# Kernel optimization log

Hardware: AMD Instinct MI355X
Metric: run time of the kernel (lower is better)

Reference implementation:

```python
import jax, jax.numpy as jnp
import numpy as np

V, DW, DH, OUT = 50000, 300, 50, 4
B, T = 1024, 200


def setup_inputs() -> dict:
    key = jax.random.key(0)
    ks = jax.random.split(key, 9)
    x = jax.random.randint(ks[0], (B, T), 0, V)
    lengs = jax.random.randint(ks[1], (B,), 1, T + 1)  # valid lengths >= 1
    k = 1.0 / np.sqrt(DH)
    emb = jax.random.normal(ks[2], (V, DW), jnp.float32)
    emb = emb.at[0].set(0.0)  # padding_idx=0
    w_ih = jax.random.uniform(ks[3], (4 * DH, DW), jnp.float32, -k, k)
    w_hh = jax.random.uniform(ks[4], (4 * DH, DH), jnp.float32, -k, k)
    b_ih = jax.random.uniform(ks[5], (4 * DH,), jnp.float32, -k, k)
    b_hh = jax.random.uniform(ks[6], (4 * DH,), jnp.float32, -k, k)
    w_out = jax.random.uniform(ks[7], (OUT, DH), jnp.float32, -k, k)
    b_out = jax.random.uniform(ks[8], (OUT,), jnp.float32, -k, k)
    return {"x": x, "lengs": lengs, "emb": emb, "w_ih": w_ih, "w_hh": w_hh,
            "b_ih": b_ih, "b_hh": b_hh, "w_out": w_out, "b_out": b_out}


def reference(x, lengs, emb, w_ih, w_hh, b_ih, b_hh, w_out, b_out):
    b, t = x.shape
    xe = emb[x]                                        # [B,T,DW]
    mask = jnp.arange(t)[None, :] < lengs[:, None]     # [B,T] valid steps
    bias = b_ih + b_hh                                 # [4*DH]

    def step(carry, inp):
        h, c = carry
        x_t, m_t = inp                                 # [B,DW], [B]
        g = x_t @ w_ih.T + h @ w_hh.T + bias           # [B,4*DH]
        i, f, gg, o = jnp.split(g, 4, axis=-1)         # torch gate order i,f,g,o
        c_new = jax.nn.sigmoid(f) * c + jax.nn.sigmoid(i) * jnp.tanh(gg)
        h_new = jax.nn.sigmoid(o) * jnp.tanh(c_new)
        m = m_t[:, None]
        # packed-sequence semantics: state frozen past each sequence's length
        return (jnp.where(m, h_new, h), jnp.where(m, c_new, c)), None

    h0 = jnp.zeros((b, DH), xe.dtype)
    (h, _), _ = jax.lax.scan(step, (h0, h0),
                             (xe.transpose(1, 0, 2), mask.T))
    logits = h @ w_out.T + b_out                       # hidden.view(B,-1) -> Linear
    return jax.nn.softmax(logits, axis=1)
```

## Files before the change

### kernel.cpp

```cpp
#include <hip/hip_runtime.h>
#include <math.h>

#define VOCAB 50000
#define DW 300
#define DH 50
#define G4 200
#define BATCH 1024
#define TMAX 200
#define OUTC 4

__global__ __launch_bounds__(256) void transpose_wih(
    const float* __restrict__ w_ih, float* __restrict__ w_T)
{
    int i = blockIdx.x * 256 + threadIdx.x;
    if (i < G4 * DW) {
        int u = i / DW, k = i % DW;
        w_T[k * G4 + u] = w_ih[i];
    }
}

__global__ __launch_bounds__(256, 2) void proj_kernel(
    const float* __restrict__ emb, const float* __restrict__ w_T,
    const float* __restrict__ b_ih, const float* __restrict__ b_hh,
    float* __restrict__ emb_proj)
{
    __shared__ __align__(16) float e_s[100 * 108];
    const int tid = threadIdx.x;
    const int v0 = blockIdx.x * 100;
    const int m_idx = tid / 25;
    const int n_idx = tid % 25;

    float acc[10][8];
#pragma unroll
    for (int m = 0; m < 10; m++)
#pragma unroll
        for (int c = 0; c < 8; c++) acc[m][c] = 0.f;

    for (int kc = 0; kc < DW; kc += 100) {
        __syncthreads();
        for (int i = tid; i < 2500; i += 256) {
            int r = i / 25, c = i % 25;
            float4 v = *(const float4*)&emb[(size_t)(v0 + r) * DW + kc + c * 4];
            *(float4*)&e_s[r * 108 + c * 4] = v;
        }
        __syncthreads();

        if (tid < 250) {
#pragma unroll 2
            for (int kk = 0; kk < 25; kk++) {
                float4 e4[10];
#pragma unroll
                for (int m = 0; m < 10; m++)
                    e4[m] = *(const float4*)&e_s[(m_idx * 10 + m) * 108 + kk * 4];
                const float* wbase = w_T + (size_t)(kc + kk * 4) * G4 + n_idx * 8;
#pragma unroll
                for (int j = 0; j < 4; j++) {
                    float4 wa = *(const float4*)(wbase + j * G4);
                    float4 wb = *(const float4*)(wbase + j * G4 + 4);
#pragma unroll
                    for (int m = 0; m < 10; m++) {
                        float ev = (j == 0) ? e4[m].x : (j == 1) ? e4[m].y
                                 : (j == 2) ? e4[m].z : e4[m].w;
                        acc[m][0] = fmaf(ev, wa.x, acc[m][0]);
                        acc[m][1] = fmaf(ev, wa.y, acc[m][1]);
                        acc[m][2] = fmaf(ev, wa.z, acc[m][2]);
                        acc[m][3] = fmaf(ev, wa.w, acc[m][3]);
                        acc[m][4] = fmaf(ev, wb.x, acc[m][4]);
                        acc[m][5] = fmaf(ev, wb.y, acc[m][5]);
                        acc[m][6] = fmaf(ev, wb.z, acc[m][6]);
                        acc[m][7] = fmaf(ev, wb.w, acc[m][7]);
                    }
                }
            }
        }
    }

    if (tid < 250) {
#pragma unroll
        for (int c = 0; c < 8; c++) {
            int u = n_idx * 8 + c;
            float bias = b_ih[u] + b_hh[u];
            int u2 = (u % DH) * 4 + (u / DH);
#pragma unroll
            for (int m = 0; m < 10; m++)
                emb_proj[(size_t)(v0 + m_idx * 10 + m) * G4 + u2] = acc[m][c] + bias;
        }
    }
}

__device__ __forceinline__ float tanh_f(float x) {
    float e2 = __expf(fminf(2.f * x, 60.f));
    return (e2 - 1.f) / (e2 + 1.f);
}

__global__ __launch_bounds__(64, 1) void lstm_kernel(
    const int* __restrict__ x, const int* __restrict__ lengs,
    const float* __restrict__ emb_proj, const float* __restrict__ w_hh,
    const float* __restrict__ w_out, const float* __restrict__ b_out,
    float* __restrict__ out)
{
    __shared__ __align__(16) float h_s[52];
    __shared__ int x_s[TMAX];
    __shared__ float red[OUTC];

    const int l  = threadIdx.x;
    const int b  = blockIdx.x;
    const int ll = (l < DH) ? l : DH - 1;
    const int len = lengs[b];

    for (int i = l; i < TMAX; i += 64) x_s[i] = x[b * TMAX + i];
    if (l < 52) h_s[l] = 0.f;

    float4 rwi[13], rwf[13], rwg[13], rwo[13];
    {
        const float* wr;
#define LOADROW(dst, gate)                                                    \
        wr = w_hh + (size_t)((gate) * DH + ll) * DH;                          \
        _Pragma("unroll")                                                     \
        for (int k4 = 0; k4 < 12; k4++) {                                     \
            float2 a = *(const float2*)(wr + 4 * k4);                         \
            float2 bb = *(const float2*)(wr + 4 * k4 + 2);                    \
            dst[k4] = make_float4(a.x, a.y, bb.x, bb.y);                      \
        }                                                                     \
        { float2 a = *(const float2*)(wr + 48);                               \
          dst[12] = make_float4(a.x, a.y, 0.f, 0.f); }
        LOADROW(rwi, 0) LOADROW(rwf, 1) LOADROW(rwg, 2) LOADROW(rwo, 3)
#undef LOADROW
    }

    float c_reg = 0.f;
    const float* ep = emb_proj;
    float4 p0 = *(const float4*)(ep + (size_t)x_s[0] * G4 + 4 * ll);
    float4 p1 = *(const float4*)(ep + (size_t)x_s[1 < TMAX ? 1 : 0] * G4 + 4 * ll);

    for (int t = 0; t < len; t++) {
        float4 cur = p0;
        p0 = p1;
        int nt = (t + 2 < TMAX) ? t + 2 : TMAX - 1;
        p1 = *(const float4*)(ep + (size_t)x_s[nt] * G4 + 4 * ll);

        float gi = cur.x, gf = cur.y, gc = cur.z, go = cur.w;
#pragma unroll
        for (int k4 = 0; k4 < 13; k4++) {
            float4 h4 = *(const float4*)&h_s[4 * k4];
            gi = fmaf(h4.x, rwi[k4].x, fmaf(h4.y, rwi[k4].y,
                 fmaf(h4.z, rwi[k4].z, fmaf(h4.w, rwi[k4].w, gi))));
            gf = fmaf(h4.x, rwf[k4].x, fmaf(h4.y, rwf[k4].y,
                 fmaf(h4.z, rwf[k4].z, fmaf(h4.w, rwf[k4].w, gf))));
            gc = fmaf(h4.x, rwg[k4].x, fmaf(h4.y, rwg[k4].y,
                 fmaf(h4.z, rwg[k4].z, fmaf(h4.w, rwg[k4].w, gc))));
            go = fmaf(h4.x, rwo[k4].x, fmaf(h4.y, rwo[k4].y,
                 fmaf(h4.z, rwo[k4].z, fmaf(h4.w, rwo[k4].w, go))));
        }
        float si = 1.f / (1.f + __expf(-gi));
        float sf = 1.f / (1.f + __expf(-gf));
        float so = 1.f / (1.f + __expf(-go));
        float cn = fmaf(sf, c_reg, si * tanh_f(gc));
        c_reg = cn;
        float hn = so * tanh_f(cn);
        if (l < DH) h_s[l] = hn;
    }

    if (l < OUTC) {
        float lg = b_out[l];
        const float* wo = w_out + l * DH;
#pragma unroll
        for (int k = 0; k < DH; k++) lg = fmaf(h_s[k], wo[k], lg);
        red[l] = lg;
    }
    if (l < OUTC) {
        float m = fmaxf(fmaxf(red[0], red[1]), fmaxf(red[2], red[3]));
        float s = 0.f;
#pragma unroll
        for (int j = 0; j < OUTC; j++) s += __expf(red[j] - m);
        out[b * OUTC + l] = __expf(red[l] - m) / s;
    }
}

extern "C" void kernel_launch(void* const* d_in, const int* in_sizes, int n_in,
                              void* d_out, int out_size, void* d_ws, size_t ws_size,
                              hipStream_t stream) {
    const int*   x     = (const int*)d_in[0];
    const int*   lengs = (const int*)d_in[1];
    const float* emb   = (const float*)d_in[2];
    const float* w_ih  = (const float*)d_in[3];
    const float* w_hh  = (const float*)d_in[4];
    const float* b_ih  = (const float*)d_in[5];
    const float* b_hh  = (const float*)d_in[6];
    const float* w_out = (const float*)d_in[7];
    const float* b_out = (const float*)d_in[8];
    float* out = (float*)d_out;

    float* emb_proj = (float*)d_ws;
    float* w_T      = emb_proj + (size_t)VOCAB * G4;

    hipLaunchKernelGGL(transpose_wih, dim3((G4 * DW + 255) / 256), dim3(256),
                       0, stream, w_ih, w_T);
    hipLaunchKernelGGL(proj_kernel, dim3(VOCAB / 100), dim3(256), 0, stream,
                       emb, w_T, b_ih, b_hh, emb_proj);
    hipLaunchKernelGGL(lstm_kernel, dim3(BATCH), dim3(64), 0, stream,
                       x, lengs, emb_proj, w_hh, w_out, b_out, out);
}
```

Baseline: 353.9 us.

## Broadcast LSTM hidden state via readlane and register-pipeline the projection GEMM

The recurrent loop now keeps h in registers and broadcasts each element with readlane, replacing the LDS write and read of h every timestep. The loop is unrolled by two with predicated updates instead of an exact-length loop. The projection GEMM drops its LDS staging and syncthreads, loads embedding rows and weights straight from global memory with double-buffered registers, and uses 80-row tiles. W_hh is also pre-laid-out into padded float4 rows by a merged prep kernel. These changes trade LDS traffic for more register pressure and more uncoalesced global loads in the GEMM.

```diff
diff --git a/kernel.cpp b/kernel.cpp
--- a/kernel.cpp
+++ b/kernel.cpp
@@ -9,14 +9,59 @@
 #define TMAX 200
 #define OUTC 4
 
-__global__ __launch_bounds__(256) void transpose_wih(
-    const float* __restrict__ w_ih, float* __restrict__ w_T)
+
+__global__ __launch_bounds__(256) void prep_kernel(
+    const float* __restrict__ w_ih, const float* __restrict__ w_hh,
+    float* __restrict__ w_T, float* __restrict__ w2)
 {
     int i = blockIdx.x * 256 + threadIdx.x;
     if (i < G4 * DW) {
         int u = i / DW, k = i % DW;
         w_T[k * G4 + u] = w_ih[i];
     }
+    int j = i - G4 * DW;
+    if (j >= 0 && j < DH * 208) {
+        int l = j / 208, r = j % 208;
+        int g = r / 52, k = r % 52;
+        w2[j] = (k < DH) ? w_hh[(g * DH + l) * DH + k] : 0.f;
+    }
+}
+
+__device__ __forceinline__ float getc(const float4& v, int kc) {
+    return kc == 0 ? v.x : kc == 1 ? v.y : kc == 2 ? v.z : v.w;
+}
+
+__device__ __forceinline__ void loade(const float* eb, int kk, float4 (&e)[8]) {
+#pragma unroll
+    for (int m = 0; m < 8; m++)
+        e[m] = *(const float4*)(eb + m * DW + kk * 4);
+}
+__device__ __forceinline__ void loadw(const float* wb, int kk,
+                                      float4 (&wa)[4], float4 (&wb4)[4]) {
+#pragma unroll
+    for (int j = 0; j < 4; j++) {
+        wa[j]  = *(const float4*)(wb + (kk * 4 + j) * G4);
+        wb4[j] = *(const float4*)(wb + (kk * 4 + j) * G4 + 4);
+    }
+}
+__device__ __forceinline__ void comp8(const float4 (&e)[8],
+                                      const float4 (&wa)[4], const float4 (&wb4)[4],
+                                      float (&acc)[8][8]) {
+#pragma unroll
+    for (int j = 0; j < 4; j++) {
+#pragma unroll
+        for (int m = 0; m < 8; m++) {
+            float ev = getc(e[m], j);
+            acc[m][0] = fmaf(ev, wa[j].x,  acc[m][0]);
+            acc[m][1] = fmaf(ev, wa[j].y,  acc[m][1]);
+            acc[m][2] = fmaf(ev, wa[j].z,  acc[m][2]);
+            acc[m][3] = fmaf(ev, wa[j].w,  acc[m][3]);
+            acc[m][4] = fmaf(ev, wb4[j].x, acc[m][4]);
+            acc[m][5] = fmaf(ev, wb4[j].y, acc[m][5]);
+            acc[m][6] = fmaf(ev, wb4[j].z, acc[m][6]);
+            acc[m][7] = fmaf(ev, wb4[j].w, acc[m][7]);
+        }
+    }
 }
 
 __global__ __launch_bounds__(256, 2) void proj_kernel(
@@ -24,67 +69,39 @@
     const float* __restrict__ b_ih, const float* __restrict__ b_hh,
     float* __restrict__ emb_proj)
 {
-    __shared__ __align__(16) float e_s[100 * 108];
     const int tid = threadIdx.x;
-    const int v0 = blockIdx.x * 100;
-    const int m_idx = tid / 25;
-    const int n_idx = tid % 25;
-
-    float acc[10][8];
-#pragma unroll
-    for (int m = 0; m < 10; m++)
+    const int tt  = (tid < 250) ? tid : 249;
+    const int m_idx = tt / 25, n_idx = tt % 25;
+    const int r0 = blockIdx.x * 80 + m_idx * 8;
+
+    const float* eb = emb + (size_t)r0 * DW;
+    const float* wb = w_T + n_idx * 8;
+
+    float acc[8][8];
+#pragma unroll
+    for (int m = 0; m < 8; m++)
 #pragma unroll
         for (int c = 0; c < 8; c++) acc[m][c] = 0.f;
 
-    for (int kc = 0; kc < DW; kc += 100) {
-        __syncthreads();
-        for (int i = tid; i < 2500; i += 256) {
-            int r = i / 25, c = i % 25;
-            float4 v = *(const float4*)&emb[(size_t)(v0 + r) * DW + kc + c * 4];
-            *(float4*)&e_s[r * 108 + c * 4] = v;
-        }
-        __syncthreads();
-
-        if (tid < 250) {
-#pragma unroll 2
-            for (int kk = 0; kk < 25; kk++) {
-                float4 e4[10];
-#pragma unroll
-                for (int m = 0; m < 10; m++)
-                    e4[m] = *(const float4*)&e_s[(m_idx * 10 + m) * 108 + kk * 4];
-                const float* wbase = w_T + (size_t)(kc + kk * 4) * G4 + n_idx * 8;
-#pragma unroll
-                for (int j = 0; j < 4; j++) {
-                    float4 wa = *(const float4*)(wbase + j * G4);
-                    float4 wb = *(const float4*)(wbase + j * G4 + 4);
-#pragma unroll
-                    for (int m = 0; m < 10; m++) {
-                        float ev = (j == 0) ? e4[m].x : (j == 1) ? e4[m].y
-                                 : (j == 2) ? e4[m].z : e4[m].w;
-                        acc[m][0] = fmaf(ev, wa.x, acc[m][0]);
-                        acc[m][1] = fmaf(ev, wa.y, acc[m][1]);
-                        acc[m][2] = fmaf(ev, wa.z, acc[m][2]);
-                        acc[m][3] = fmaf(ev, wa.w, acc[m][3]);
-                        acc[m][4] = fmaf(ev, wb.x, acc[m][4]);
-                        acc[m][5] = fmaf(ev, wb.y, acc[m][5]);
-                        acc[m][6] = fmaf(ev, wb.z, acc[m][6]);
-                        acc[m][7] = fmaf(ev, wb.w, acc[m][7]);
-                    }
-                }
-            }
-        }
-    }
-
-    if (tid < 250) {
-#pragma unroll
-        for (int c = 0; c < 8; c++) {
-            int u = n_idx * 8 + c;
-            float bias = b_ih[u] + b_hh[u];
-            int u2 = (u % DH) * 4 + (u / DH);
-#pragma unroll
-            for (int m = 0; m < 10; m++)
-                emb_proj[(size_t)(v0 + m_idx * 10 + m) * G4 + u2] = acc[m][c] + bias;
-        }
+    float4 eC[8], eN[8], wCa[4], wCb[4], wNa[4], wNb[4];
+    loade(eb, 0, eC); loadw(wb, 0, wCa, wCb);
+
+    for (int k4 = 0; k4 < 74; k4 += 2) {
+        loade(eb, k4 + 1, eN); loadw(wb, k4 + 1, wNa, wNb);
+        comp8(eC, wCa, wCb, acc);
+        loade(eb, k4 + 2, eC); loadw(wb, k4 + 2, wCa, wCb);
+        comp8(eN, wNa, wNb, acc);
+    }
+    comp8(eC, wCa, wCb, acc);
+
+#pragma unroll
+    for (int c = 0; c < 8; c++) {
+        int u = n_idx * 8 + c;
+        float bias = b_ih[u] + b_hh[u];
+        int u2 = (u % DH) * 4 + (u / DH);
+#pragma unroll
+        for (int m = 0; m < 8; m++)
+            emb_proj[(size_t)(r0 + m) * G4 + u2] = acc[m][c] + bias;
     }
 }
 
@@ -93,15 +110,39 @@
     return (e2 - 1.f) / (e2 + 1.f);
 }
 
+__device__ __forceinline__ void lstm_step(float4 cur, int tt, int len,
+                                          const float4 (&w4)[4][13],
+                                          float& hn, float& c) {
+    float gi = cur.x, gf = cur.y, gc = cur.z, go = cur.w;
+#pragma unroll
+    for (int k = 0; k < DH; k++) {
+        float hk = __uint_as_float(
+            __builtin_amdgcn_readlane(__float_as_uint(hn), k));
+        const int k4 = k >> 2, kc = k & 3;
+        gi = fmaf(hk, getc(w4[0][k4], kc), gi);
+        gf = fmaf(hk, getc(w4[1][k4], kc), gf);
+        gc = fmaf(hk, getc(w4[2][k4], kc), gc);
+        go = fmaf(hk, getc(w4[3][k4], kc), go);
+    }
+    float si = 1.f / (1.f + __expf(-gi));
+    float sf = 1.f / (1.f + __expf(-gf));
+    float so = 1.f / (1.f + __expf(-go));
+    float cn = fmaf(sf, c, si * tanh_f(gc));
+    float hh = so * tanh_f(cn);
+    bool act = tt < len;
+    c  = act ? cn : c;
+    hn = act ? hh : hn;
+}
+
 __global__ __launch_bounds__(64, 1) void lstm_kernel(
     const int* __restrict__ x, const int* __restrict__ lengs,
-    const float* __restrict__ emb_proj, const float* __restrict__ w_hh,
+    const float* __restrict__ emb_proj, const float* __restrict__ w2,
     const float* __restrict__ w_out, const float* __restrict__ b_out,
     float* __restrict__ out)
 {
-    __shared__ __align__(16) float h_s[52];
+    __shared__ float h_fin[DH];
+    __shared__ float red[OUTC];
     __shared__ int x_s[TMAX];
-    __shared__ float red[OUTC];
 
     const int l  = threadIdx.x;
     const int b  = blockIdx.x;
@@ -109,65 +150,48 @@
     const int len = lengs[b];
 
     for (int i = l; i < TMAX; i += 64) x_s[i] = x[b * TMAX + i];
-    if (l < 52) h_s[l] = 0.f;
-
-    float4 rwi[13], rwf[13], rwg[13], rwo[13];
+
+    float4 w4[4][13];
     {
-        const float* wr;
-#define LOADROW(dst, gate)                                                    \
-        wr = w_hh + (size_t)((gate) * DH + ll) * DH;                          \
-        _Pragma("unroll")                                                     \
-        for (int k4 = 0; k4 < 12; k4++) {                                     \
-            float2 a = *(const float2*)(wr + 4 * k4);                         \
-            float2 bb = *(const float2*)(wr + 4 * k4 + 2);                    \
-            dst[k4] = make_float4(a.x, a.y, bb.x, bb.y);                      \
-        }                                                                     \
-        { float2 a = *(const float2*)(wr + 48);                               \
-          dst[12] = make_float4(a.x, a.y, 0.f, 0.f); }
-        LOADROW(rwi, 0) LOADROW(rwf, 1) LOADROW(rwg, 2) LOADROW(rwo, 3)
-#undef LOADROW
-    }
-
-    float c_reg = 0.f;
-    const float* ep = emb_proj;
-    float4 p0 = *(const float4*)(ep + (size_t)x_s[0] * G4 + 4 * ll);
-    float4 p1 = *(const float4*)(ep + (size_t)x_s[1 < TMAX ? 1 : 0] * G4 + 4 * ll);
-
-    for (int t = 0; t < len; t++) {
-        float4 cur = p0;
-        p0 = p1;
-        int nt = (t + 2 < TMAX) ? t + 2 : TMAX - 1;
-        p1 = *(const float4*)(ep + (size_t)x_s[nt] * G4 + 4 * ll);
-
-        float gi = cur.x, gf = cur.y, gc = cur.z, go = cur.w;
-#pragma unroll
-        for (int k4 = 0; k4 < 13; k4++) {
-            float4 h4 = *(const float4*)&h_s[4 * k4];
-            gi = fmaf(h4.x, rwi[k4].x, fmaf(h4.y, rwi[k4].y,
-                 fmaf(h4.z, rwi[k4].z, fmaf(h4.w, rwi[k4].w, gi))));
-            gf = fmaf(h4.x, rwf[k4].x, fmaf(h4.y, rwf[k4].y,
-                 fmaf(h4.z, rwf[k4].z, fmaf(h4.w, rwf[k4].w, gf))));
-            gc = fmaf(h4.x, rwg[k4].x, fmaf(h4.y, rwg[k4].y,
-                 fmaf(h4.z, rwg[k4].z, fmaf(h4.w, rwg[k4].w, gc))));
-            go = fmaf(h4.x, rwo[k4].x, fmaf(h4.y, rwo[k4].y,
-                 fmaf(h4.z, rwo[k4].z, fmaf(h4.w, rwo[k4].w, go))));
-        }
-        float si = 1.f / (1.f + __expf(-gi));
-        float sf = 1.f / (1.f + __expf(-gf));
-        float so = 1.f / (1.f + __expf(-go));
-        float cn = fmaf(sf, c_reg, si * tanh_f(gc));
-        c_reg = cn;
-        float hn = so * tanh_f(cn);
-        if (l < DH) h_s[l] = hn;
-    }
+        const float4* wp = (const float4*)w2 + ll * 52;
+#pragma unroll
+        for (int g = 0; g < 4; g++)
+#pragma unroll
+            for (int k4 = 0; k4 < 13; k4++) w4[g][k4] = wp[g * 13 + k4];
+    }
+    __syncthreads();
+
+    const float* ep = emb_proj + 4 * ll;
+    float hn = 0.f, c = 0.f;
+    float4 pA = *(const float4*)(ep + (size_t)x_s[0] * G4);
+    float4 pB = *(const float4*)(ep + (size_t)x_s[1] * G4);
+
+    const int T2 = (len + 1) & ~1;
+    for (int t = 0; t < T2; t += 2) {
+        int n2 = (t + 2 < TMAX) ? t + 2 : TMAX - 1;
+        int n3 = (t + 3 < TMAX) ? t + 3 : TMAX - 1;
+        int tok2 = x_s[n2], tok3 = x_s[n3];
+
+        float4 curA = pA;
+        pA = *(const float4*)(ep + (size_t)tok2 * G4);
+        lstm_step(curA, t, len, w4, hn, c);
+
+        float4 curB = pB;
+        pB = *(const float4*)(ep + (size_t)tok3 * G4);
+        lstm_step(curB, t + 1, len, w4, hn, c);
+    }
+
+    if (l < DH) h_fin[l] = hn;
+    __syncthreads();
 
     if (l < OUTC) {
         float lg = b_out[l];
         const float* wo = w_out + l * DH;
 #pragma unroll
-        for (int k = 0; k < DH; k++) lg = fmaf(h_s[k], wo[k], lg);
+        for (int k = 0; k < DH; k++) lg = fmaf(h_fin[k], wo[k], lg);
         red[l] = lg;
     }
+    __syncthreads();
     if (l < OUTC) {
         float m = fmaxf(fmaxf(red[0], red[1]), fmaxf(red[2], red[3]));
         float s = 0.f;
@@ -193,11 +217,12 @@
 
     float* emb_proj = (float*)d_ws;
     float* w_T      = emb_proj + (size_t)VOCAB * G4;
-
-    hipLaunchKernelGGL(transpose_wih, dim3((G4 * DW + 255) / 256), dim3(256),
-                       0, stream, w_ih, w_T);
-    hipLaunchKernelGGL(proj_kernel, dim3(VOCAB / 100), dim3(256), 0, stream,
+    float* w2       = w_T + (size_t)DW * G4;
+
+    hipLaunchKernelGGL(prep_kernel, dim3((G4 * DW + DH * 208 + 255) / 256),
+                       dim3(256), 0, stream, w_ih, w_hh, w_T, w2);
+    hipLaunchKernelGGL(proj_kernel, dim3(VOCAB / 80), dim3(256), 0, stream,
                        emb, w_T, b_ih, b_hh, emb_proj);
     hipLaunchKernelGGL(lstm_kernel, dim3(BATCH), dim3(64), 0, stream,
-                       x, lengs, emb_proj, w_hh, w_out, b_out, out);
-}
+                       x, lengs, emb_proj, w2, w_out, b_out, out);
+}
```

Result: slower. 505.3 us (+42.8%).
